# Optimization experiments

Measured on AMD Instinct MI355X. Metric: run time of the kernel, lower is better.

## Reference

```python
import jax, jax.numpy as jnp
import numpy as np

CH = 512      # channels
CI = CH // 4  # in_channel = 128
DILS = (1, 4, 8, 12)
GN_GROUPS = 32


def conv2d(x, w, dil=1, pad=0):
    # x: (N,Cin,H,W), w: (Cout,Cin,kh,kw)
    return jax.lax.conv_general_dilated(
        x, w, window_strides=(1, 1), padding=[(pad, pad), (pad, pad)],
        rhs_dilation=(dil, dil),
        dimension_numbers=('NCHW', 'OIHW', 'NCHW'))


def group_norm(x, gamma, beta, groups=GN_GROUPS, eps=1e-5):
    N, C, H, W = x.shape
    xg = x.reshape(N, groups, C // groups, H, W)
    mu = jnp.mean(xg, axis=(2, 3, 4), keepdims=True)
    var = jnp.var(xg, axis=(2, 3, 4), keepdims=True)
    xn = ((xg - mu) * jax.lax.rsqrt(var + eps)).reshape(N, C, H, W)
    return xn * gamma[None, :, None, None] + beta[None, :, None, None]


def dyn_branch(xd, w_cat, d):
    # dynamic filter: (N, 9, H, W), softmax over the K=9 taps per pixel
    f = jax.nn.softmax(conv2d(xd, w_cat, dil=d, pad=d), axis=1)
    N, C, H, W = xd.shape
    xp = jnp.pad(xd, ((0, 0), (0, 0), (d, d), (d, d)))
    # fused unfold + weighted sum: accumulate 9 shifted views * per-pixel weight
    out = jnp.zeros_like(xd)
    k = 0
    for i in range(3):
        for j in range(3):
            out = out + xp[:, :, i * d:i * d + H, j * d:j * d + W] * f[:, k:k + 1]
            k += 1
    return out


def setup_inputs():
    key = jax.random.key(0)
    ks = jax.random.split(key, 16)
    s = 0.05
    return {
        'x': jax.random.normal(ks[0], (4, CH, 128, 128), jnp.float32),
        'w_scale1': jax.random.normal(ks[1], (CI, CH, 1, 1), jnp.float32) * s,
        'gn1_g': jnp.ones((CI,), jnp.float32),
        'gn1_b': jnp.zeros((CI,), jnp.float32),
        'w_cata': jax.random.normal(ks[2], (9, CI, 3, 3), jnp.float32) * s,
        'w_catb': jax.random.normal(ks[3], (9, CI, 3, 3), jnp.float32) * s,
        'w_catc': jax.random.normal(ks[4], (9, CI, 3, 3), jnp.float32) * s,
        'w_catd': jax.random.normal(ks[5], (9, CI, 3, 3), jnp.float32) * s,
        'w_scale2': jax.random.normal(ks[6], (CI, 5 * CI, 1, 1), jnp.float32) * s,
        'gn2_g': jnp.ones((CI,), jnp.float32),
        'gn2_b': jnp.zeros((CI,), jnp.float32),
        'w_scale3': jax.random.normal(ks[7], (CH, CI, 1, 1), jnp.float32) * s,
        'gn3_g': jnp.ones((CH,), jnp.float32),
        'gn3_b': jnp.zeros((CH,), jnp.float32),
    }


def reference(x, w_scale1, gn1_g, gn1_b, w_cata, w_catb, w_catc, w_catd,
              w_scale2, gn2_g, gn2_b, w_scale3, gn3_g, gn3_b):
    # scale1: 1x1 conv -> GN -> ReLU
    xd = jax.nn.relu(group_norm(conv2d(x, w_scale1), gn1_g, gn1_b))
    # four dilated dynamic-filter branches (unfold + softmax-weighted reduce)
    outs = [dyn_branch(xd, w, d)
            for w, d in zip((w_cata, w_catb, w_catc, w_catd), DILS)]
    cat = jnp.concatenate([xd] + outs, axis=1)  # (N, 5*CI, H, W)
    y = jax.nn.relu(group_norm(conv2d(cat, w_scale2), gn2_g, gn2_b))
    y = jax.nn.relu(group_norm(conv2d(y, w_scale3), gn3_g, gn3_b))
    return y
```

## Files before the change

kernel.cpp:

```cpp
#include <hip/hip_runtime.h>
#include <math.h>

#define HW 16384

typedef float f32x4 __attribute__((ext_vector_type(4)));
typedef __bf16 bf16x8 __attribute__((ext_vector_type(8)));
typedef unsigned short u16x4 __attribute__((ext_vector_type(4)));
typedef unsigned short u16x8 __attribute__((ext_vector_type(8)));

__device__ __forceinline__ unsigned short f2bf(float f) {
  unsigned u = __float_as_uint(f);
  u += 0x7fffu + ((u >> 16) & 1u);
  return (unsigned short)(u >> 16);
}
__device__ __forceinline__ float bf2f(unsigned short s) {
  return __uint_as_float(((unsigned)s) << 16);
}

__global__ void prep_kernel(const float* __restrict__ w1, const float* __restrict__ w2,
                            const float* __restrict__ w3,
                            const float* __restrict__ wa, const float* __restrict__ wb,
                            const float* __restrict__ wc, const float* __restrict__ wd,
                            unsigned short* __restrict__ w1b, unsigned short* __restrict__ w2b,
                            unsigned short* __restrict__ w3b, unsigned short* __restrict__ wr) {
  int idx = blockIdx.x * 256 + threadIdx.x;
  if (idx < 65536) { w1b[idx] = f2bf(w1[idx]); }
  else if (idx < 147456) { int j = idx - 65536; w2b[j] = f2bf(w2[j]); }
  else if (idx < 212992) { int j = idx - 147456; w3b[j] = f2bf(w3[j]); }
  else if (idx < 286720) {
    int j = idx - 212992;
    int br = j / 18432, rem = j % 18432;
    int tap = rem / 2048, rem2 = rem % 2048;
    int kt = rem2 / 128, c = rem2 % 128;
    const float* w = (br == 0) ? wa : (br == 1) ? wb : (br == 2) ? wc : wd;
    float v = (kt < 9) ? w[(kt * 128 + c) * 9 + tap] : 0.f;
    wr[j] = f2bf(v);
  }
}

__device__ __forceinline__ void gn_partial_epilogue(
    f32x4 (&acc)[8], int wv, int lane, int t, int n, int blkx,
    float* __restrict__ part, float (*ps)[32], float (*pss)[32]) {
  float gs[8], gss[8];
#pragma unroll
  for (int cb = 0; cb < 8; ++cb) {
    float s = 0.f, ss = 0.f;
#pragma unroll
    for (int r = 0; r < 4; ++r) { float v = acc[cb][r]; s += v; ss += v * v; }
#pragma unroll
    for (int m = 0; m < 4; ++m) {
      const int msk[4] = {1, 2, 16, 32};
      s += __shfl_xor(s, msk[m]); ss += __shfl_xor(ss, msk[m]);
    }
    gs[cb] = s; gss[cb] = ss;
  }
  if (lane < 16 && (lane & 3) == 0) {
    int q = lane >> 2;
#pragma unroll
    for (int cb = 0; cb < 8; ++cb) { ps[wv][cb * 4 + q] = gs[cb]; pss[wv][cb * 4 + q] = gss[cb]; }
  }
  __syncthreads();
  if (t < 32) {
    float a = ps[0][t] + ps[1][t] + ps[2][t] + ps[3][t];
    float b = pss[0][t] + pss[1][t] + pss[2][t] + pss[3][t];
    float* pp = part + ((size_t)(n * 32 + t) * 256 + blkx) * 2;
    pp[0] = a; pp[1] = b;
  }
}

__global__ __launch_bounds__(256) void conv1f_kernel(
    const float* __restrict__ x, const unsigned short* __restrict__ w1b,
    unsigned short* __restrict__ outb, float* __restrict__ part) {
  __shared__ float xs[2][64][65];
  __shared__ float ps[4][32], pss[4][32];
  int t = threadIdx.x;
  int wv = t >> 6, lane = t & 63, lr = lane & 15, lg = lane >> 4;
  int n = blockIdx.y;
  int p0 = blockIdx.x * 64;
  const float* xn = x + (size_t)n * 512 * HW + p0;
  f32x4 acc[8];
#pragma unroll
  for (int cb = 0; cb < 8; ++cb) acc[cb] = (f32x4){0.f, 0.f, 0.f, 0.f};

  int ci_l = t >> 4, px4 = (t & 15) * 4;
  float4 r[4];

#pragma unroll
  for (int pass = 0; pass < 4; ++pass)
    r[pass] = *(const float4*)(xn + (size_t)(pass * 16 + ci_l) * HW + px4);
#pragma unroll
  for (int pass = 0; pass < 4; ++pass) {
    int cl = pass * 16 + ci_l;
    xs[0][cl][px4 + 0] = r[pass].x; xs[0][cl][px4 + 1] = r[pass].y;
    xs[0][cl][px4 + 2] = r[pass].z; xs[0][cl][px4 + 3] = r[pass].w;
  }

  for (int kt = 0; kt < 8; ++kt) {
    int cur = kt & 1;
    if (kt < 7) {
#pragma unroll
      for (int pass = 0; pass < 4; ++pass)
        r[pass] = *(const float4*)(xn + (size_t)((kt + 1) * 64 + pass * 16 + ci_l) * HW + px4);
    }
    __syncthreads();
#pragma unroll
    for (int ks = 0; ks < 2; ++ks) {
      bf16x8 a;
#pragma unroll
      for (int j = 0; j < 8; ++j) {
        unsigned short us = f2bf(xs[cur][ks * 32 + lg * 8 + j][wv * 16 + lr]);
        a[j] = *(__bf16*)&us;
      }
#pragma unroll
      for (int cb = 0; cb < 8; ++cb) {
        bf16x8 b = *(const bf16x8*)(w1b + (size_t)(cb * 16 + lr) * 512
                                    + kt * 64 + ks * 32 + lg * 8);
        acc[cb] = __builtin_amdgcn_mfma_f32_16x16x32_bf16(a, b, acc[cb], 0, 0, 0);
      }
    }
    if (kt < 7) {
#pragma unroll
      for (int pass = 0; pass < 4; ++pass) {
        int cl = pass * 16 + ci_l;
        xs[cur ^ 1][cl][px4 + 0] = r[pass].x; xs[cur ^ 1][cl][px4 + 1] = r[pass].y;
        xs[cur ^ 1][cl][px4 + 2] = r[pass].z; xs[cur ^ 1][cl][px4 + 3] = r[pass].w;
      }
    }
  }
  unsigned short* on = outb + (size_t)n * HW * 640;
#pragma unroll
  for (int cb = 0; cb < 8; ++cb)
#pragma unroll
    for (int r2 = 0; r2 < 4; ++r2)
      on[(size_t)(p0 + wv * 16 + lg * 4 + r2) * 640 + cb * 16 + lr] = f2bf(acc[cb][r2]);
  __syncthreads();
  gn_partial_epilogue(acc, wv, lane, t, n, blockIdx.x, part, ps, pss);
}

template<int K>
__global__ __launch_bounds__(256) void conv_pm_kernel(
    const unsigned short* __restrict__ act, const unsigned short* __restrict__ w,
    unsigned short* __restrict__ outb, float* __restrict__ part, int ldd) {
  __shared__ float ps[4][32], pss[4][32];
  int t = threadIdx.x;
  int wv = t >> 6, lane = t & 63;
  int lr = lane & 15, lg = lane >> 4;
  int n = blockIdx.y;
  int p0 = blockIdx.x * 64 + wv * 16;
  const unsigned short* an = act + (size_t)n * HW * K;
  f32x4 acc[8];
#pragma unroll
  for (int cb = 0; cb < 8; ++cb) acc[cb] = (f32x4){0.f, 0.f, 0.f, 0.f};
  const unsigned short* ap = an + (size_t)(p0 + lr) * K + lg * 8;
  const unsigned short* bp = w + (size_t)lr * K + lg * 8;
  for (int ks = 0; ks < K / 32; ++ks) {
    bf16x8 a = *(const bf16x8*)(ap + ks * 32);
#pragma unroll
    for (int cb = 0; cb < 8; ++cb) {
      bf16x8 b = *(const bf16x8*)(bp + (size_t)cb * 16 * K + ks * 32);
      acc[cb] = __builtin_amdgcn_mfma_f32_16x16x32_bf16(a, b, acc[cb], 0, 0, 0);
    }
  }
  unsigned short* on = outb + (size_t)n * HW * ldd;
#pragma unroll
  for (int cb = 0; cb < 8; ++cb)
#pragma unroll
    for (int r = 0; r < 4; ++r)
      on[(size_t)(p0 + lg * 4 + r) * ldd + cb * 16 + lr] = f2bf(acc[cb][r]);
  gn_partial_epilogue(acc, wv, lane, t, n, blockIdx.x, part, ps, pss);
}

__global__ void gnf256_kernel(const float* __restrict__ part, float* __restrict__ stats) {
  int t = threadIdx.x;
  float s = 0.f, ss = 0.f;
  for (int b = 0; b < 256; ++b) {
    const float* pp = part + ((size_t)t * 256 + b) * 2;
    s += pp[0]; ss += pp[1];
  }
  float inv = 1.f / (4.f * HW);
  float mean = s * inv, var = ss * inv - mean * mean;
  stats[2 * t] = mean; stats[2 * t + 1] = rsqrtf(var + 1e-5f);
}

__global__ __launch_bounds__(256) void gna_ip_kernel(
    unsigned short* __restrict__ dst, const float* __restrict__ stats,
    const float* __restrict__ gamma, const float* __restrict__ beta, int ldd) {
  int idx = blockIdx.x * 256 + threadIdx.x;
  int g = idx & 31;
  int p = (idx >> 5) & (HW - 1);
  int n = idx >> 19;
  unsigned short* ptr = dst + ((size_t)n * HW + p) * ldd + 4 * g;
  u16x4 v = *(u16x4*)ptr;
  int sg = n * 32 + g;
  float mean = stats[2 * sg], rstd = stats[2 * sg + 1];
  float sc0 = rstd * gamma[4 * g + 0], sc1 = rstd * gamma[4 * g + 1];
  float sc2 = rstd * gamma[4 * g + 2], sc3 = rstd * gamma[4 * g + 3];
  float sh0 = beta[4 * g + 0] - mean * sc0, sh1 = beta[4 * g + 1] - mean * sc1;
  float sh2 = beta[4 * g + 2] - mean * sc2, sh3 = beta[4 * g + 3] - mean * sc3;
  u16x4 o;
  o[0] = f2bf(fmaxf(fmaf(bf2f(v[0]), sc0, sh0), 0.f));
  o[1] = f2bf(fmaxf(fmaf(bf2f(v[1]), sc1, sh1), 0.f));
  o[2] = f2bf(fmaxf(fmaf(bf2f(v[2]), sc2, sh2), 0.f));
  o[3] = f2bf(fmaxf(fmaf(bf2f(v[3]), sc3, sh3), 0.f));
  *(u16x4*)ptr = o;
}

__global__ __launch_bounds__(256) void conv3_kernel(
    const unsigned short* __restrict__ y, const unsigned short* __restrict__ w3,
    unsigned short* __restrict__ outb, float* __restrict__ part) {
  int wv = threadIdx.x >> 6, lane = threadIdx.x & 63;
  int lr = lane & 15, lg = lane >> 4;
  int n = blockIdx.y, zc = blockIdx.z;
  int co0 = zc * 128 + wv * 32;
  int p0 = blockIdx.x * 128;
  const unsigned short* yn = y + (size_t)n * HW * 128;
  f32x4 acc[2][8];
#pragma unroll
  for (int pr = 0; pr < 2; ++pr)
#pragma unroll
    for (int cb = 0; cb < 8; ++cb) acc[pr][cb] = (f32x4){0.f, 0.f, 0.f, 0.f};
#pragma unroll
  for (int ks = 0; ks < 4; ++ks) {
    bf16x8 a0 = *(const bf16x8*)(w3 + (size_t)(co0 + lr) * 128 + ks * 32 + lg * 8);
    bf16x8 a1 = *(const bf16x8*)(w3 + (size_t)(co0 + 16 + lr) * 128 + ks * 32 + lg * 8);
#pragma unroll
    for (int cb = 0; cb < 8; ++cb) {
      bf16x8 b = *(const bf16x8*)(yn + (size_t)(p0 + cb * 16 + lr) * 128 + ks * 32 + lg * 8);
      acc[0][cb] = __builtin_amdgcn_mfma_f32_16x16x32_bf16(a0, b, acc[0][cb], 0, 0, 0);
      acc[1][cb] = __builtin_amdgcn_mfma_f32_16x16x32_bf16(a1, b, acc[1][cb], 0, 0, 0);
    }
  }
  unsigned short* on = outb + (size_t)n * 512 * HW;
  float s[2] = {0.f, 0.f}, ss[2] = {0.f, 0.f};
#pragma unroll
  for (int pr = 0; pr < 2; ++pr)
#pragma unroll
    for (int cb = 0; cb < 8; ++cb)
#pragma unroll
      for (int r = 0; r < 4; ++r) {
        float v = acc[pr][cb][r];
        on[(size_t)(co0 + pr * 16 + lg * 4 + r) * HW + p0 + cb * 16 + lr] = f2bf(v);
        s[pr] += v; ss[pr] += v * v;
      }
#pragma unroll
  for (int pr = 0; pr < 2; ++pr) {
    float a = s[pr], b = ss[pr];
    for (int m = 1; m < 64; m <<= 1) { a += __shfl_xor(a, m); b += __shfl_xor(b, m); }
    if (lane == 0) {
      float* pp = part + ((((size_t)n * 4 + zc) * 128 + blockIdx.x) * 8 + wv * 2 + pr) * 2;
      pp[0] = a; pp[1] = b;
    }
  }
}

__global__ void gnf3_kernel(const float* __restrict__ part, float* __restrict__ stats) {
  int t = threadIdx.x;
  int n = t >> 5, g = t & 31;
  int zc = g >> 3, sub = g & 7;
  float s = 0.f, ss = 0.f;
  for (int xb = 0; xb < 128; ++xb) {
    const float* pp = part + ((((size_t)n * 4 + zc) * 128 + xb) * 8 + sub) * 2;
    s += pp[0]; ss += pp[1];
  }
  float inv = 1.f / (16.f * HW);
  float mean = s * inv, var = ss * inv - mean * mean;
  stats[2 * t] = mean; stats[2 * t + 1] = rsqrtf(var + 1e-5f);
}

__global__ __launch_bounds__(256) void gn3_apply_kernel(
    const unsigned short* __restrict__ y3b, const float* __restrict__ stats,
    const float* __restrict__ gamma, const float* __restrict__ beta,
    float* __restrict__ out) {
  size_t e8 = ((size_t)blockIdx.x * 256 + threadIdx.x) * 8;
  int n = (int)(e8 >> 23);
  int c = (int)((e8 >> 14) & 511);
  int sg = n * 32 + (c >> 4);
  float mean = stats[2 * sg], rstd = stats[2 * sg + 1];
  float scale = rstd * gamma[c];
  float shift = beta[c] - mean * scale;
  u16x8 u = *(const u16x8*)(y3b + e8);
  float4 o0, o1;
  o0.x = fmaxf(fmaf(bf2f(u[0]), scale, shift), 0.f);
  o0.y = fmaxf(fmaf(bf2f(u[1]), scale, shift), 0.f);
  o0.z = fmaxf(fmaf(bf2f(u[2]), scale, shift), 0.f);
  o0.w = fmaxf(fmaf(bf2f(u[3]), scale, shift), 0.f);
  o1.x = fmaxf(fmaf(bf2f(u[4]), scale, shift), 0.f);
  o1.y = fmaxf(fmaf(bf2f(u[5]), scale, shift), 0.f);
  o1.z = fmaxf(fmaf(bf2f(u[6]), scale, shift), 0.f);
  o1.w = fmaxf(fmaf(bf2f(u[7]), scale, shift), 0.f);
  *(float4*)(out + e8) = o0;
  *(float4*)(out + e8 + 4) = o1;
}

#define DP 136

__global__ __launch_bounds__(512, 4) void dynfused6_kernel(
    const unsigned short* __restrict__ cat, const unsigned short* __restrict__ wr,
    unsigned short* __restrict__ catw) {
  extern __shared__ char smem[];
  unsigned short* rowbuf = (unsigned short*)smem;
  float* fl = (float*)(smem + 3 * 88 * DP * 2);
  int t = threadIdx.x;
  int bid = blockIdx.x;
  int rh = ((bid & 7) << 5) + (bid >> 3);
  int row = rh >> 1, hw = rh & 1;
  int n = blockIdx.y >> 2, br = blockIdx.y & 3;
  int d = (br == 0) ? 1 : 4 * br;
  const unsigned short* xb = cat + (size_t)n * HW * 640;

  int rg[3] = { max(row - d, 0), row, min(row + d, 127) };
  bool rv[3] = { row - d >= 0, true, row + d < 128 };
  int cbase = hw * 64 - 12;

  {
    u16x8 vreg[9];
#pragma unroll
    for (int k = 0; k < 9; ++k) {
      int ci = t + (k << 9);
      if (k == 8 && ci >= 4224) continue;
      int s = (ci >= 2816) ? 2 : (ci >= 1408 ? 1 : 0);
      int rem = ci - s * 1408;
      int slot = rem >> 4, c = rem & 15;
      int gcol = min(max(cbase + slot, 0), 127);
      vreg[k] = *(const u16x8*)(xb + ((size_t)(rg[s] * 128 + gcol)) * 640 + c * 8);
    }
#pragma unroll
    for (int k = 0; k < 9; ++k) {
      int ci = t + (k << 9);
      if (k == 8 && ci >= 4224) continue;
      int s = (ci >= 2816) ? 2 : (ci >= 1408 ? 1 : 0);
      int rem = ci - s * 1408;
      int slot = rem >> 4, c = rem & 15;
      *(u16x8*)(rowbuf + ((size_t)s * 88 + slot) * DP + c * 8) = vreg[k];
    }
  }
  __syncthreads();

  if (t < 256) {
    int wv = t >> 6, lane = t & 63;
    int lr = lane & 15, lg = lane >> 4;
    const unsigned short* wb = wr + (size_t)br * 9 * 16 * 128;
    const bf16x8 zb = {(__bf16)0.f, (__bf16)0.f, (__bf16)0.f, (__bf16)0.f,
                       (__bf16)0.f, (__bf16)0.f, (__bf16)0.f, (__bf16)0.f};
    f32x4 acc = (f32x4){0.f, 0.f, 0.f, 0.f};
    int pxl = wv * 16 + lr;
    int gw = hw * 64 + pxl;
#pragma unroll
    for (int tap = 0; tap < 9; ++tap) {
      int s = tap / 3;
      int dw = (tap % 3 - 1) * d;
      int slot = 12 + pxl + dw;
      bool val = rv[s] && ((unsigned)(gw + dw) < 128u);
      const unsigned short* ap = rowbuf + ((size_t)s * 88 + slot) * DP + lg * 8;
      const unsigned short* wt = wb + (size_t)(tap * 16 + lr) * 128 + lg * 8;
#pragma unroll
      for (int ks = 0; ks < 4; ++ks) {
        bf16x8 a = *(const bf16x8*)(ap + ks * 32);
        if (!val) a = zb;
        bf16x8 b = *(const bf16x8*)(wt + ks * 32);
        acc = __builtin_amdgcn_mfma_f32_16x16x32_bf16(a, b, acc, 0, 0, 0);
      }
    }
#pragma unroll
    for (int r = 0; r < 4; ++r) {
      float v = acc[r];
      float m = (lr < 9) ? v : -3.0e38f;
#pragma unroll
      for (int msk = 1; msk < 16; msk <<= 1) m = fmaxf(m, __shfl_xor(m, msk));
      float e = (lr < 9) ? expf(v - m) : 0.f;
      float su = e;
#pragma unroll
      for (int msk = 1; msk < 16; msk <<= 1) su += __shfl_xor(su, msk);
      fl[(wv * 16 + lg * 4 + r) * 17 + lr] = e / su;
    }
  }
  __syncthreads();

  {
    int pxl = t >> 3, c8 = t & 7;
    int gw = hw * 64 + pxl;
    float oacc[16];
#pragma unroll
    for (int i = 0; i < 16; ++i) oacc[i] = 0.f;
#pragma unroll
    for (int tap = 0; tap < 9; ++tap) {
      int s = tap / 3;
      int dw = (tap % 3 - 1) * d;
      int slot = 12 + pxl + dw;
      bool val = rv[s] && ((unsigned)(gw + dw) < 128u);
      float f = val ? fl[pxl * 17 + tap] : 0.f;
      const unsigned short* ap = rowbuf + ((size_t)s * 88 + slot) * DP + c8 * 16;
#pragma unroll
      for (int cc = 0; cc < 2; ++cc) {
        u16x8 u = *(const u16x8*)(ap + cc * 8);
#pragma unroll
        for (int i = 0; i < 8; ++i)
          oacc[cc * 8 + i] = fmaf(f, bf2f(u[i]), oacc[cc * 8 + i]);
      }
    }
    unsigned short* orow = catw + ((size_t)n * HW + row * 128 + gw) * 640
                           + 128 * (br + 1) + c8 * 16;
#pragma unroll
    for (int cc = 0; cc < 2; ++cc) {
      u16x8 o;
#pragma unroll
      for (int i = 0; i < 8; ++i) o[i] = f2bf(oacc[cc * 8 + i]);
      *(u16x8*)(orow + cc * 8) = o;
    }
  }
}

extern "C" void kernel_launch(void* const* d_in, const int* in_sizes, int n_in,
                              void* d_out, int out_size, void* d_ws, size_t ws_size,
                              hipStream_t stream) {
  const float* x   = (const float*)d_in[0];
  const float* w1  = (const float*)d_in[1];
  const float* g1  = (const float*)d_in[2];
  const float* b1  = (const float*)d_in[3];
  const float* wca = (const float*)d_in[4];
  const float* wcb = (const float*)d_in[5];
  const float* wcc = (const float*)d_in[6];
  const float* wcd = (const float*)d_in[7];
  const float* w2  = (const float*)d_in[8];
  const float* g2  = (const float*)d_in[9];
  const float* b2  = (const float*)d_in[10];
  const float* w3  = (const float*)d_in[11];
  const float* g3  = (const float*)d_in[12];
  const float* b3  = (const float*)d_in[13];
  float* out = (float*)d_out;

  float* ws = (float*)d_ws;
  unsigned short* cat = (unsigned short*)(ws + 25165824);
  unsigned short* y2b = (unsigned short*)(ws + 8388608);
  unsigned short* y3b = (unsigned short*)(ws + 25165824);
  float* aux = ws + 46137344;
  unsigned short* w1b = (unsigned short*)(aux);
  unsigned short* w2b = (unsigned short*)(aux + 32768);
  unsigned short* w3b = (unsigned short*)(aux + 73728);
  unsigned short* wr  = (unsigned short*)(aux + 106496);
  float* part  = aux + 143360;
  float* part3 = aux + 208896;
  float* st1   = aux + 241664;
  float* st2   = aux + 241920;
  float* st3   = aux + 242176;

  dim3 blk(256);
  const int dynLds = 3 * 88 * DP * 2 + 64 * 17 * 4;
  (void)hipFuncSetAttribute((const void*)dynfused6_kernel,
                            hipFuncAttributeMaxDynamicSharedMemorySize, dynLds);

  prep_kernel<<<dim3(1120), blk, 0, stream>>>(w1, w2, w3, wca, wcb, wcc, wcd,
                                              w1b, w2b, w3b, wr);

  conv1f_kernel<<<dim3(256, 4), blk, 0, stream>>>(x, w1b, cat, part);
  gnf256_kernel<<<dim3(1), dim3(128), 0, stream>>>(part, st1);
  gna_ip_kernel<<<dim3(8192), blk, 0, stream>>>(cat, st1, g1, b1, 640);

  dynfused6_kernel<<<dim3(256, 16), dim3(512), dynLds, stream>>>(cat, wr, cat);

  conv_pm_kernel<640><<<dim3(256, 4), blk, 0, stream>>>(cat, w2b, y2b, part, 128);
  gnf256_kernel<<<dim3(1), dim3(128), 0, stream>>>(part, st2);
  gna_ip_kernel<<<dim3(8192), blk, 0, stream>>>(y2b, st2, g2, b2, 128);

  conv3_kernel<<<dim3(128, 4, 4), blk, 0, stream>>>(y2b, w3b, y3b, part3);
  gnf3_kernel<<<dim3(1), dim3(128), 0, stream>>>(part3, st3);
  gn3_apply_kernel<<<dim3(16384), blk, 0, stream>>>(y3b, st3, g3, b3, out);
}
```

Before: 372.7 us.

## Transpose conv1 LDS tile, unroll pm conv loop, parallelize GN finalize reductions

Result: slower. 384.5 us (+3.2%).

```diff
diff --git a/kernel.cpp b/kernel.cpp
--- a/kernel.cpp
+++ b/kernel.cpp
@@ -71,7 +71,7 @@
 __global__ __launch_bounds__(256) void conv1f_kernel(
     const float* __restrict__ x, const unsigned short* __restrict__ w1b,
     unsigned short* __restrict__ outb, float* __restrict__ part) {
-  __shared__ float xs[2][64][65];
+  __shared__ float xs[2][64][68];
   __shared__ float ps[4][32], pss[4][32];
   int t = threadIdx.x;
   int wv = t >> 6, lane = t & 63, lr = lane & 15, lg = lane >> 4;
@@ -91,8 +91,8 @@
 #pragma unroll
   for (int pass = 0; pass < 4; ++pass) {
     int cl = pass * 16 + ci_l;
-    xs[0][cl][px4 + 0] = r[pass].x; xs[0][cl][px4 + 1] = r[pass].y;
-    xs[0][cl][px4 + 2] = r[pass].z; xs[0][cl][px4 + 3] = r[pass].w;
+    xs[0][px4 + 0][cl] = r[pass].x; xs[0][px4 + 1][cl] = r[pass].y;
+    xs[0][px4 + 2][cl] = r[pass].z; xs[0][px4 + 3][cl] = r[pass].w;
   }
 
   for (int kt = 0; kt < 8; ++kt) {
@@ -105,12 +105,15 @@
     __syncthreads();
 #pragma unroll
     for (int ks = 0; ks < 2; ++ks) {
+      const float* arow = &xs[cur][wv * 16 + lr][ks * 32 + lg * 8];
+      float4 a0 = *(const float4*)arow;
+      float4 a1 = *(const float4*)(arow + 4);
       bf16x8 a;
-#pragma unroll
-      for (int j = 0; j < 8; ++j) {
-        unsigned short us = f2bf(xs[cur][ks * 32 + lg * 8 + j][wv * 16 + lr]);
-        a[j] = *(__bf16*)&us;
-      }
+      unsigned short us;
+      us = f2bf(a0.x); a[0] = *(__bf16*)&us; us = f2bf(a0.y); a[1] = *(__bf16*)&us;
+      us = f2bf(a0.z); a[2] = *(__bf16*)&us; us = f2bf(a0.w); a[3] = *(__bf16*)&us;
+      us = f2bf(a1.x); a[4] = *(__bf16*)&us; us = f2bf(a1.y); a[5] = *(__bf16*)&us;
+      us = f2bf(a1.z); a[6] = *(__bf16*)&us; us = f2bf(a1.w); a[7] = *(__bf16*)&us;
 #pragma unroll
       for (int cb = 0; cb < 8; ++cb) {
         bf16x8 b = *(const bf16x8*)(w1b + (size_t)(cb * 16 + lr) * 512
@@ -122,8 +125,8 @@
 #pragma unroll
       for (int pass = 0; pass < 4; ++pass) {
         int cl = pass * 16 + ci_l;
-        xs[cur ^ 1][cl][px4 + 0] = r[pass].x; xs[cur ^ 1][cl][px4 + 1] = r[pass].y;
-        xs[cur ^ 1][cl][px4 + 2] = r[pass].z; xs[cur ^ 1][cl][px4 + 3] = r[pass].w;
+        xs[cur ^ 1][px4 + 0][cl] = r[pass].x; xs[cur ^ 1][px4 + 1][cl] = r[pass].y;
+        xs[cur ^ 1][px4 + 2][cl] = r[pass].z; xs[cur ^ 1][px4 + 3][cl] = r[pass].w;
       }
     }
   }
@@ -153,6 +156,7 @@
   for (int cb = 0; cb < 8; ++cb) acc[cb] = (f32x4){0.f, 0.f, 0.f, 0.f};
   const unsigned short* ap = an + (size_t)(p0 + lr) * K + lg * 8;
   const unsigned short* bp = w + (size_t)lr * K + lg * 8;
+#pragma unroll 2
   for (int ks = 0; ks < K / 32; ++ks) {
     bf16x8 a = *(const bf16x8*)(ap + ks * 32);
 #pragma unroll
@@ -170,16 +174,26 @@
   gn_partial_epilogue(acc, wv, lane, t, n, blockIdx.x, part, ps, pss);
 }
 
-__global__ void gnf256_kernel(const float* __restrict__ part, float* __restrict__ stats) {
+__global__ __launch_bounds__(1024) void gnf256_kernel(
+    const float* __restrict__ part, float* __restrict__ stats) {
+  __shared__ float sh[1024], sh2[1024];
   int t = threadIdx.x;
+  int tg = t >> 3, sub = t & 7;
   float s = 0.f, ss = 0.f;
-  for (int b = 0; b < 256; ++b) {
-    const float* pp = part + ((size_t)t * 256 + b) * 2;
+  for (int b = sub * 32; b < sub * 32 + 32; ++b) {
+    const float* pp = part + ((size_t)tg * 256 + b) * 2;
     s += pp[0]; ss += pp[1];
   }
-  float inv = 1.f / (4.f * HW);
-  float mean = s * inv, var = ss * inv - mean * mean;
-  stats[2 * t] = mean; stats[2 * t + 1] = rsqrtf(var + 1e-5f);
+  sh[t] = s; sh2[t] = ss;
+  __syncthreads();
+  if (t < 128) {
+    float a = 0.f, b2 = 0.f;
+#pragma unroll
+    for (int i = 0; i < 8; ++i) { a += sh[t * 8 + i]; b2 += sh2[t * 8 + i]; }
+    float inv = 1.f / (4.f * HW);
+    float mean = a * inv, var = b2 * inv - mean * mean;
+    stats[2 * t] = mean; stats[2 * t + 1] = rsqrtf(var + 1e-5f);
+  }
 }
 
 __global__ __launch_bounds__(256) void gna_ip_kernel(
@@ -253,18 +267,28 @@
   }
 }
 
-__global__ void gnf3_kernel(const float* __restrict__ part, float* __restrict__ stats) {
+__global__ __launch_bounds__(1024) void gnf3_kernel(
+    const float* __restrict__ part, float* __restrict__ stats) {
+  __shared__ float sh[1024], sh2[1024];
   int t = threadIdx.x;
-  int n = t >> 5, g = t & 31;
+  int e = t >> 3, xbs = t & 7;
+  int n = e >> 5, g = e & 31;
   int zc = g >> 3, sub = g & 7;
   float s = 0.f, ss = 0.f;
-  for (int xb = 0; xb < 128; ++xb) {
+  for (int xb = xbs * 16; xb < xbs * 16 + 16; ++xb) {
     const float* pp = part + ((((size_t)n * 4 + zc) * 128 + xb) * 8 + sub) * 2;
     s += pp[0]; ss += pp[1];
   }
-  float inv = 1.f / (16.f * HW);
-  float mean = s * inv, var = ss * inv - mean * mean;
-  stats[2 * t] = mean; stats[2 * t + 1] = rsqrtf(var + 1e-5f);
+  sh[t] = s; sh2[t] = ss;
+  __syncthreads();
+  if (t < 128) {
+    float a = 0.f, b2 = 0.f;
+#pragma unroll
+    for (int i = 0; i < 8; ++i) { a += sh[t * 8 + i]; b2 += sh2[t * 8 + i]; }
+    float inv = 1.f / (16.f * HW);
+    float mean = a * inv, var = b2 * inv - mean * mean;
+    stats[2 * t] = mean; stats[2 * t + 1] = rsqrtf(var + 1e-5f);
+  }
 }
 
 __global__ __launch_bounds__(256) void gn3_apply_kernel(
@@ -453,16 +477,16 @@
                                               w1b, w2b, w3b, wr);
 
   conv1f_kernel<<<dim3(256, 4), blk, 0, stream>>>(x, w1b, cat, part);
-  gnf256_kernel<<<dim3(1), dim3(128), 0, stream>>>(part, st1);
+  gnf256_kernel<<<dim3(1), dim3(1024), 0, stream>>>(part, st1);
   gna_ip_kernel<<<dim3(8192), blk, 0, stream>>>(cat, st1, g1, b1, 640);
 
   dynfused6_kernel<<<dim3(256, 16), dim3(512), dynLds, stream>>>(cat, wr, cat);
 
   conv_pm_kernel<640><<<dim3(256, 4), blk, 0, stream>>>(cat, w2b, y2b, part, 128);
-  gnf256_kernel<<<dim3(1), dim3(128), 0, stream>>>(part, st2);
+  gnf256_kernel<<<dim3(1), dim3(1024), 0, stream>>>(part, st2);
   gna_ip_kernel<<<dim3(8192), blk, 0, stream>>>(y2b, st2, g2, b2, 128);
 
   conv3_kernel<<<dim3(128, 4, 4), blk, 0, stream>>>(y2b, w3b, y3b, part3);
-  gnf3_kernel<<<dim3(1), dim3(128), 0, stream>>>(part3, st3);
+  gnf3_kernel<<<dim3(1), dim3(1024), 0, stream>>>(part3, st3);
   gn3_apply_kernel<<<dim3(16384), blk, 0, stream>>>(y3b, st3, g3, b3, out);
 }
```
